# Optimization experiments

Hardware: AMD Instinct MI355X
Metric: run time of the kernel (lower is better)

## Reference

```python
import jax, jax.numpy as jnp
import numpy as np

B = 2097152
C = 10  # CIFAR-10 classes, hardcoded via `for j in range(10)` in the original


def setup_inputs() -> dict:
    key = jax.random.key(0)
    k1, k2, k3 = jax.random.split(key, 3)
    inp = jax.random.normal(k1, (B, C), dtype=jnp.float32)
    distance_matrix = jax.random.uniform(k2, (C, C), dtype=jnp.float32)
    target = jax.random.randint(k3, (B,), 0, C, dtype=jnp.int64)
    return {"input": inp, "distance_matrix": distance_matrix, "target": target}


def reference(input, distance_matrix, target):
    # distance_vector[i] = distance_matrix[target[i]]  -> [B, C]
    dv = distance_matrix[target]
    # distance_rank = argsort indices of each row (index of j-th smallest), as float
    r = jnp.argsort(dv, axis=1).astype(jnp.float32)  # [B, C]
    rt = jnp.take_along_axis(r, target[:, None], axis=1)  # [B, 1] rank entry at target position
    margins = jnp.maximum(0.0, 1.0 + r - rt)  # [B, C]
    mask = jnp.arange(C)[None, :] != target[:, None]  # exclude j == target[i]
    ranking_loss = jnp.sum(jnp.where(mask, margins, 0.0))
    # cross_entropy with mean reduction
    logp = jax.nn.log_softmax(input, axis=1)
    ce = -jnp.mean(jnp.take_along_axis(logp, target[:, None], axis=1))
    return ce + ranking_loss / input.shape[0]
```

## Files before the change

kernel.cpp:

```cpp
#include <hip/hip_runtime.h>

#define THREADS 256
#define BLOCKS  2048

__device__ __forceinline__ float row_loss(
    float a0, float a1, float a2, float a3, float a4,
    float a5, float a6, float a7, float a8, float a9,
    int t, const float* __restrict__ smargin)
{
    float m = fmaxf(fmaxf(fmaxf(a0, a1), fmaxf(a2, a3)),
                    fmaxf(fmaxf(fmaxf(a4, a5), fmaxf(a6, a7)), fmaxf(a8, a9)));
    float e0 = __expf(a0 - m), e1 = __expf(a1 - m);
    float e2 = __expf(a2 - m), e3 = __expf(a3 - m);
    float e4 = __expf(a4 - m), e5 = __expf(a5 - m);
    float e6 = __expf(a6 - m), e7 = __expf(a7 - m);
    float e8 = __expf(a8 - m), e9 = __expf(a9 - m);
    float s = ((e0 + e1) + (e2 + e3)) + (((e4 + e5) + (e6 + e7)) + (e8 + e9));
    float xt = a0;
    xt = (t == 1) ? a1 : xt;
    xt = (t == 2) ? a2 : xt;
    xt = (t == 3) ? a3 : xt;
    xt = (t == 4) ? a4 : xt;
    xt = (t == 5) ? a5 : xt;
    xt = (t == 6) ? a6 : xt;
    xt = (t == 7) ? a7 : xt;
    xt = (t == 8) ? a8 : xt;
    xt = (t == 9) ? a9 : xt;
    return m + __logf(s) - xt + smargin[t];
}

__global__ __launch_bounds__(THREADS) void ranking_loss_kernel(
    const float* __restrict__ input,
    const float* __restrict__ dm,
    const int* __restrict__ target,
    float* __restrict__ out,
    int B)
{
    __shared__ float  smargin[10];
    __shared__ float  swsum[THREADS / 64];
    __shared__ float4 stage[THREADS * 5];

    if (threadIdx.x < 10) {
        int t = threadIdx.x;
        float row[10];
        #pragma unroll
        for (int k = 0; k < 10; ++k) row[k] = dm[t * 10 + k];
        int rt = 0;
        #pragma unroll
        for (int k = 0; k < 10; ++k) {
            int cnt = 0;
            #pragma unroll
            for (int mi = 0; mi < 10; ++mi)
                cnt += (row[mi] < row[k]) || (row[mi] == row[k] && mi < k);
            if (cnt == t) rt = k;
        }
        float f = (float)(10 - rt);
        smargin[t] = 0.5f * f * (f + 1.0f) - 1.0f;
    }
    __syncthreads();

    const int nPairs = B >> 1;
    const int stride = gridDim.x * THREADS;
    const int tid = threadIdx.x;
    float acc = 0.0f;

    for (int p0 = blockIdx.x * THREADS; p0 < nPairs; p0 += stride) {
        const int p = p0 + tid;
        if (p0 + THREADS <= nPairs) {
            const float4* gsrc = (const float4*)input + (size_t)p0 * 5;
            float4 r0 = gsrc[0 * THREADS + tid];
            float4 r1 = gsrc[1 * THREADS + tid];
            float4 r2 = gsrc[2 * THREADS + tid];
            float4 r3 = gsrc[3 * THREADS + tid];
            float4 r4 = gsrc[4 * THREADS + tid];
            int2 tt = ((const int2*)target)[p];

            __syncthreads();
            stage[0 * THREADS + tid] = r0;
            stage[1 * THREADS + tid] = r1;
            stage[2 * THREADS + tid] = r2;
            stage[3 * THREADS + tid] = r3;
            stage[4 * THREADS + tid] = r4;
            __syncthreads();

            const float4* rp = &stage[tid * 5];
            float4 q0 = rp[0], q1 = rp[1], q2 = rp[2], q3 = rp[3], q4 = rp[4];

            acc += row_loss(q0.x, q0.y, q0.z, q0.w, q1.x, q1.y, q1.z, q1.w,
                            q2.x, q2.y, tt.x, smargin);
            acc += row_loss(q2.z, q2.w, q3.x, q3.y, q3.z, q3.w, q4.x, q4.y,
                            q4.z, q4.w, tt.y, smargin);
        } else if (p < nPairs) {
            const float* x = input + (size_t)p * 20;
            int t0 = target[2 * p], t1 = target[2 * p + 1];
            acc += row_loss(x[0], x[1], x[2], x[3], x[4],
                            x[5], x[6], x[7], x[8], x[9], t0, smargin);
            acc += row_loss(x[10], x[11], x[12], x[13], x[14],
                            x[15], x[16], x[17], x[18], x[19], t1, smargin);
        }
    }

    #pragma unroll
    for (int off = 32; off > 0; off >>= 1)
        acc += __shfl_down(acc, off, 64);
    const int lane = threadIdx.x & 63;
    const int wave = threadIdx.x >> 6;
    if (lane == 0) swsum[wave] = acc;
    __syncthreads();
    if (threadIdx.x == 0) {
        float b = 0.0f;
        #pragma unroll
        for (int w = 0; w < THREADS / 64; ++w) b += swsum[w];
        atomicAdd(out, b * (1.0f / (float)B));
    }
}

extern "C" void kernel_launch(void* const* d_in, const int* in_sizes, int n_in,
                              void* d_out, int out_size, void* d_ws, size_t ws_size,
                              hipStream_t stream) {
    const float* input  = (const float*)d_in[0];
    const float* dm     = (const float*)d_in[1];
    const int*   target = (const int*)d_in[2];
    float* out = (float*)d_out;

    const int B = in_sizes[0] / 10;

    ranking_loss_kernel<<<BLOCKS, THREADS, 0, stream>>>(input, dm, target, out, B);
}
```

Measured before the change: 137.3 us.

## Drop LDS staging and grid-stride loop; launch one thread per row pair

Removes the shared-memory transpose that gave coalesced float4 loads, and has each thread read its own 80-byte pair of rows directly with strided float4 loads. The persistent grid-stride loop is replaced by a grid sized to cover all pairs, one pair per thread. The aim is to avoid the two block barriers and the LDS traffic per iteration. In exchange, global loads become uncoalesced, there are many more blocks, and each block issues its own atomicAdd.

```diff
diff --git a/kernel.cpp b/kernel.cpp
--- a/kernel.cpp
+++ b/kernel.cpp
@@ -1,7 +1,6 @@
 #include <hip/hip_runtime.h>
 
 #define THREADS 256
-#define BLOCKS  2048
 
 __device__ __forceinline__ float row_loss(
     float a0, float a1, float a2, float a3, float a4,
@@ -36,9 +35,8 @@
     float* __restrict__ out,
     int B)
 {
-    __shared__ float  smargin[10];
-    __shared__ float  swsum[THREADS / 64];
-    __shared__ float4 stage[THREADS * 5];
+    __shared__ float smargin[10];
+    __shared__ float swsum[THREADS / 64];
 
     if (threadIdx.x < 10) {
         int t = threadIdx.x;
@@ -60,44 +58,18 @@
     __syncthreads();
 
     const int nPairs = B >> 1;
-    const int stride = gridDim.x * THREADS;
-    const int tid = threadIdx.x;
+    const int p = blockIdx.x * THREADS + threadIdx.x;
     float acc = 0.0f;
 
-    for (int p0 = blockIdx.x * THREADS; p0 < nPairs; p0 += stride) {
-        const int p = p0 + tid;
-        if (p0 + THREADS <= nPairs) {
-            const float4* gsrc = (const float4*)input + (size_t)p0 * 5;
-            float4 r0 = gsrc[0 * THREADS + tid];
-            float4 r1 = gsrc[1 * THREADS + tid];
-            float4 r2 = gsrc[2 * THREADS + tid];
-            float4 r3 = gsrc[3 * THREADS + tid];
-            float4 r4 = gsrc[4 * THREADS + tid];
-            int2 tt = ((const int2*)target)[p];
+    if (p < nPairs) {
+        const float4* rp = (const float4*)input + (size_t)p * 5;
+        float4 q0 = rp[0], q1 = rp[1], q2 = rp[2], q3 = rp[3], q4 = rp[4];
+        int2 tt = ((const int2*)target)[p];
 
-            __syncthreads();
-            stage[0 * THREADS + tid] = r0;
-            stage[1 * THREADS + tid] = r1;
-            stage[2 * THREADS + tid] = r2;
-            stage[3 * THREADS + tid] = r3;
-            stage[4 * THREADS + tid] = r4;
-            __syncthreads();
-
-            const float4* rp = &stage[tid * 5];
-            float4 q0 = rp[0], q1 = rp[1], q2 = rp[2], q3 = rp[3], q4 = rp[4];
-
-            acc += row_loss(q0.x, q0.y, q0.z, q0.w, q1.x, q1.y, q1.z, q1.w,
-                            q2.x, q2.y, tt.x, smargin);
-            acc += row_loss(q2.z, q2.w, q3.x, q3.y, q3.z, q3.w, q4.x, q4.y,
-                            q4.z, q4.w, tt.y, smargin);
-        } else if (p < nPairs) {
-            const float* x = input + (size_t)p * 20;
-            int t0 = target[2 * p], t1 = target[2 * p + 1];
-            acc += row_loss(x[0], x[1], x[2], x[3], x[4],
-                            x[5], x[6], x[7], x[8], x[9], t0, smargin);
-            acc += row_loss(x[10], x[11], x[12], x[13], x[14],
-                            x[15], x[16], x[17], x[18], x[19], t1, smargin);
-        }
+        acc  = row_loss(q0.x, q0.y, q0.z, q0.w, q1.x, q1.y, q1.z, q1.w,
+                        q2.x, q2.y, tt.x, smargin);
+        acc += row_loss(q2.z, q2.w, q3.x, q3.y, q3.z, q3.w, q4.x, q4.y,
+                        q4.z, q4.w, tt.y, smargin);
     }
 
     #pragma unroll
@@ -124,6 +96,8 @@
     float* out = (float*)d_out;
 
     const int B = in_sizes[0] / 10;
+    const int nPairs = B >> 1;
+    const int blocks = (nPairs + THREADS - 1) / THREADS;
 
-    ranking_loss_kernel<<<BLOCKS, THREADS, 0, stream>>>(input, dm, target, out, B);
+    ranking_loss_kernel<<<blocks, THREADS, 0, stream>>>(input, dm, target, out, B);
 }
```

Measured after the change: 159.0 us. 15.8% more time.
